# Performance work log

Measured on AMD Instinct MI355X. Metric: run time of the kernel, lower is better.

The kernel has to match this reference:

```python
import jax, jax.numpy as jnp
import numpy as np

B, IMG, D, HEADS, L, PC, PF, OUT = 8, 128, 128, 4, 2, 8, 4, 32
HC = IMG // PC; NC = HC * HC          # 16x16 -> 256 coarse tokens
HF = IMG // PF; NF = HF * HF          # 32x32 -> 1024 fine tokens


def _ln(x, g, b):
    m = x.mean(-1, keepdims=True)
    v = x.var(-1, keepdims=True)
    return (x - m) * jax.lax.rsqrt(v + 1e-5) * g + b


def _conv(x, w, b, pad):
    y = jax.lax.conv_general_dilated(x, w, (1, 1), ((pad, pad), (pad, pad)),
                                     dimension_numbers=('NCHW', 'OIHW', 'NCHW'))
    return y + b[None, :, None, None]


def _bilinear_ac(x, oh, ow):  # F.interpolate(mode='bilinear', align_corners=True)
    _, _, H, W = x.shape
    ys = jnp.linspace(0.0, H - 1.0, oh)
    xs = jnp.linspace(0.0, W - 1.0, ow)
    y0 = jnp.floor(ys).astype(jnp.int32); y1 = jnp.minimum(y0 + 1, H - 1); wy = (ys - y0)[:, None]
    x0 = jnp.floor(xs).astype(jnp.int32); x1 = jnp.minimum(x0 + 1, W - 1); wx = (xs - x0)[None, :]
    g = lambda yi, xi: x[:, :, yi][:, :, :, xi]
    return (g(y0, x0) * (1 - wy) * (1 - wx) + g(y0, x1) * (1 - wy) * wx
            + g(y1, x0) * wy * (1 - wx) + g(y1, x1) * wy * wx)


def _patchify(x, p):  # F.unfold with kernel=stride=p, in_chans=1
    b, _, h, w = x.shape
    return x.reshape(b, h // p, p, w // p, p).transpose(0, 1, 3, 2, 4).reshape(b, (h // p) * (w // p), p * p)


def _forward(x, Wpc, bpc, Wpf, bpf, type_embed, ln1_g, ln1_b, Wqkv, Wo, bo,
             ln2_g, ln2_b, W1, b1, W2, b2, dWc, dbc, dWf, dbf, fW1, fb1, fW2, fb2):
    Bx = x.shape[0]
    # ---- multi-scale patch embed ----
    coarse = _patchify(x, PC) @ Wpc + bpc + type_embed[0]   # [B,NC,D]
    fine = _patchify(x, PF) @ Wpf + bpf                     # [B,NF,D]
    # ---- edge map: sobel -> avgpool(4) -> threshold at per-image mean ----
    gray = x.mean(1, keepdims=True)
    kx = jnp.array([[[[-1, 0, 1], [-2, 0, 2], [-1, 0, 1]]]], x.dtype)
    ky = jnp.array([[[[-1, -2, -1], [0, 0, 0], [1, 2, 1]]]], x.dtype)
    sx = _conv(gray, kx, jnp.zeros((1,), x.dtype), 1)
    sy = _conv(gray, ky, jnp.zeros((1,), x.dtype), 1)
    e = jnp.sqrt(sx ** 2 + sy ** 2)
    e = e.reshape(Bx, 1, IMG // 4, 4, IMG // 4, 4).mean((3, 5))  # [B,1,32,32] == fine grid
    mask_flat = (e > e.mean((2, 3), keepdims=True)).reshape(Bx, NF)
    # ---- static-shape analogue of per-sample masked gather + pad_sequence:
    # stable sort puts edge tokens first (original pixel order preserved), pads are zeros
    order = jnp.argsort(jnp.logical_not(mask_flat), axis=1, stable=True)   # [B,NF]
    mask_sorted = jnp.take_along_axis(mask_flat, order, 1)
    fine_sorted = jnp.take_along_axis(fine, order[..., None], 1) * mask_sorted[..., None]
    fine_sorted = fine_sorted + type_embed[1]   # type embed added to pads too (as in torch)
    tokens = jnp.concatenate([coarse, fine_sorted], axis=1)   # [B,N,D]
    N = NC + NF
    hd = D // HEADS
    scale = hd ** -0.5
    # ---- encoder blocks (pre-LN attn + MLP, irregular-token path) ----
    for l in range(L):
        y = _ln(tokens, ln1_g[l], ln1_b[l])
        qkv = (y @ Wqkv[l]).reshape(Bx, N, 3, HEADS, hd).transpose(2, 0, 3, 1, 4)
        q, k, v = qkv[0], qkv[1], qkv[2]
        attn = jax.nn.softmax(jnp.einsum('bhqd,bhkd->bhqk', q, k) * scale, axis=-1)
        o = jnp.einsum('bhqk,bhkd->bhqd', attn, v).transpose(0, 2, 1, 3).reshape(Bx, N, D)
        tokens = tokens + o @ Wo[l] + bo[l]
        y = _ln(tokens, ln2_g[l], ln2_b[l])
        tokens = tokens + jax.nn.gelu(y @ W1[l] + b1[l], approximate=False) @ W2[l] + b2[l]
    # ---- multi-scale decoder ----
    c = (tokens[:, :NC] @ dWc + dbc).reshape(Bx, HC, HC, 1).transpose(0, 3, 1, 2)
    c_up = _bilinear_ac(c, OUT, OUT)
    feats = (tokens[:, NC:] @ dWf + dbf) * mask_sorted[..., None]   # pads stay zero
    inv = jnp.argsort(order, axis=1)                                # scatter back to pixel order
    f_flat = jnp.take_along_axis(feats, inv[..., None], 1)          # [B,NF,1]
    f_map = f_flat.reshape(Bx, HF, HF, 1).transpose(0, 3, 1, 2)
    f_up = _bilinear_ac(f_map, OUT, OUT)
    fused = jnp.concatenate([c_up, f_up], axis=1)
    h = jax.nn.relu(_conv(fused, fW1, fb1, 1))
    return _conv(h, fW2, fb2, 1)   # [B,1,32,32]


def setup_inputs() -> dict:
    key = jax.random.key(0)
    ks = jax.random.split(key, 16)
    n = lambda k, shape: jax.random.normal(k, shape, jnp.float32) * 0.02
    z = lambda *shape: jnp.zeros(shape, jnp.float32)
    return {
        'x': jax.random.normal(ks[0], (B, 1, IMG, IMG), jnp.float32),
        'Wpc': n(ks[1], (PC * PC, D)), 'bpc': z(D),
        'Wpf': n(ks[2], (PF * PF, D)), 'bpf': z(D),
        'type_embed': n(ks[3], (2, D)),
        'ln1_g': jnp.ones((L, D), jnp.float32), 'ln1_b': z(L, D),
        'Wqkv': n(ks[4], (L, D, 3 * D)),
        'Wo': n(ks[5], (L, D, D)), 'bo': z(L, D),
        'ln2_g': jnp.ones((L, D), jnp.float32), 'ln2_b': z(L, D),
        'W1': n(ks[6], (L, D, 2 * D)), 'b1': z(L, 2 * D),
        'W2': n(ks[7], (L, 2 * D, D)), 'b2': z(L, D),
        'dWc': n(ks[8], (D, 1)), 'dbc': z(1),
        'dWf': n(ks[9], (D, 1)), 'dbf': z(1),
        'fW1': n(ks[10], (2, 2, 3, 3)) * 10.0, 'fb1': z(2),
        'fW2': n(ks[11], (1, 2, 3, 3)) * 10.0, 'fb2': z(1),
    }


def reference(x, Wpc, bpc, Wpf, bpf, type_embed, ln1_g, ln1_b, Wqkv, Wo, bo,
              ln2_g, ln2_b, W1, b1, W2, b2, dWc, dbc, dWf, dbf, fW1, fb1, fW2, fb2):
    return _forward(x, Wpc, bpc, Wpf, bpf, type_embed, ln1_g, ln1_b, Wqkv, Wo, bo,
                    ln2_g, ln2_b, W1, b1, W2, b2, dWc, dbc, dWf, dbf, fW1, fb1, fW2, fb2)
```

## Files before the change

kernel.cpp:

```cpp
#include <hip/hip_runtime.h>
#include <math.h>

#define Bx 8
#define IMG 128
#define DD 128
#define HEADS 4
#define LL 2
#define PCc 8
#define PFf 4
#define HCc 16
#define NCc 256
#define HFf 32
#define NFf 1024
#define NTOK 1280
#define HD 32
#define SPLIT 2
#define NSTG 10
#define NQT 20

typedef __attribute__((ext_vector_type(8))) short short8;
typedef __attribute__((ext_vector_type(4))) float f32x4;

__device__ __forceinline__ short f2bf(float f) {
  unsigned u = __builtin_bit_cast(unsigned, f);
  u += 0x7FFF + ((u >> 16) & 1);
  return (short)(u >> 16);
}
__device__ __forceinline__ float bf2f(short s) {
  unsigned u = ((unsigned)(unsigned short)s) << 16;
  return __builtin_bit_cast(float, u);
}

__global__ __launch_bounds__(256) void k_prologue(const float* __restrict__ x,
    const float* __restrict__ Wpc, const float* __restrict__ bpc,
    const float* __restrict__ Wpf, const float* __restrict__ bpf,
    const float* __restrict__ te,
    const float* __restrict__ Wqkv, const float* __restrict__ Wo,
    const float* __restrict__ W1, const float* __restrict__ W2,
    short* __restrict__ WtQKV, short* __restrict__ WtO,
    short* __restrict__ Wt1, short* __restrict__ Wt2,
    float* __restrict__ e, float* __restrict__ tokens,
    float* __restrict__ fineb) {
  int blk = blockIdx.x;
  int t = threadIdx.x;
  if (blk < 1024) {
    int idx = blk * 256 + t;
    int l = idx / 131072, r = idx % 131072;
    const float* src; short* dst; int N, off;
    if (r < 49152)      { src = Wqkv + l * 49152; dst = WtQKV + l * 49152; N = 384; off = r; }
    else if (r < 65536) { src = Wo + l * 16384;  dst = WtO + l * 16384;  N = 128; off = r - 49152; }
    else if (r < 98304) { src = W1 + l * 32768;  dst = Wt1 + l * 32768;  N = 256; off = r - 65536; }
    else                { src = W2 + l * 32768;  dst = Wt2 + l * 32768;  N = 128; off = r - 98304; }
    int k = off / N, n = off % N;
    int K = (r >= 98304) ? 256 : 128;
    dst[(size_t)n * K + k] = f2bf(src[off]);
  } else if (blk < 1536) {
    int bt = blk - 1024;
    int b = bt >> 6, tile = bt & 63;
    int ty = tile >> 3, tx = tile & 7;
    int ly = t >> 4, lx = t & 15;
    int py = ty * 16 + ly, px = tx * 16 + lx;
    const float* img = x + (size_t)b * IMG * IMG;
    float v[3][3];
    #pragma unroll
    for (int ky = 0; ky < 3; ++ky)
      #pragma unroll
      for (int kx = 0; kx < 3; ++kx) {
        int yy = py + ky - 1, xx = px + kx - 1;
        v[ky][kx] = (yy >= 0 && yy < IMG && xx >= 0 && xx < IMG)
                        ? img[yy * IMG + xx] : 0.f;
      }
    float gx = -v[0][0] + v[0][2] - 2.f * v[1][0] + 2.f * v[1][2] - v[2][0] + v[2][2];
    float gy = -v[0][0] - 2.f * v[0][1] - v[0][2] + v[2][0] + 2.f * v[2][1] + v[2][2];
    __shared__ float sm[256];
    sm[t] = sqrtf(gx * gx + gy * gy);
    __syncthreads();
    if (t < 16) {
      int cy = t >> 2, cx = t & 3;
      float s = 0.f;
      #pragma unroll
      for (int dy = 0; dy < 4; ++dy)
        #pragma unroll
        for (int dx = 0; dx < 4; ++dx) s += sm[(cy * 4 + dy) * 16 + cx * 4 + dx];
      e[b * NFf + (ty * 4 + cy) * 32 + tx * 4 + cx] = s * (1.f / 16.f);
    }
  } else if (blk < 2560) {
    int bt = (blk - 1536) * 2 + (t >> 7);
    int b = bt / NCc, tok = bt % NCc;
    int hc = tok / HCc, wc = tok % HCc;
    int half = t >> 7, d = t & 127;
    __shared__ float patch[2][PCc * PCc];
    if (d < PCc * PCc) {
      int pi = d / PCc, pj = d % PCc;
      patch[half][d] = x[(b * IMG + hc * PCc + pi) * IMG + wc * PCc + pj];
    }
    __syncthreads();
    float acc = bpc[d] + te[d];
    #pragma unroll 8
    for (int i = 0; i < PCc * PCc; ++i) acc += patch[half][i] * Wpc[i * DD + d];
    tokens[(size_t)(b * NTOK + tok) * DD + d] = acc;
  } else {
    int ft = (blk - 2560) * 2 + (t >> 7);
    int b = ft >> 10, tloc = ft & 1023;
    int hf = tloc >> 5, wf = tloc & 31;
    int half = t >> 7, d = t & 127;
    __shared__ float patch[2][PFf * PFf];
    if (d < PFf * PFf) {
      int pi = d / PFf, pj = d % PFf;
      patch[half][d] = x[(b * IMG + hf * PFf + pi) * IMG + wf * PFf + pj];
    }
    __syncthreads();
    float acc = bpf[d];
    #pragma unroll
    for (int i = 0; i < PFf * PFf; ++i) acc += patch[half][i] * Wpf[i * DD + d];
    fineb[(size_t)(b * NFf + tloc) * DD + d] = acc;
  }
}

__global__ __launch_bounds__(1024) void k_edge_sort(const float* __restrict__ e,
    int* __restrict__ order, float* __restrict__ msort) {
  int b = blockIdx.x;
  int t = threadIdx.x;
  int lane = t & 63, wave = t >> 6;
  float ev = e[b * NFf + t];
  __shared__ float wsum[16];
  __shared__ int wcnt[16];
  float r = ev;
  #pragma unroll
  for (int o = 32; o > 0; o >>= 1) r += __shfl_xor(r, o, 64);
  if (lane == 0) wsum[wave] = r;
  __syncthreads();
  float tot = 0.f;
  #pragma unroll
  for (int i = 0; i < 16; ++i) tot += wsum[i];
  float mean = tot * (1.f / 1024.f);
  int m = (ev > mean) ? 1 : 0;
  unsigned long long bal = __ballot(m);
  if (lane == 0) wcnt[wave] = __popcll(bal);
  __syncthreads();
  int wbase = 0, total = 0;
  #pragma unroll
  for (int i = 0; i < 16; ++i) {
    int c = wcnt[i];
    if (i < wave) wbase += c;
    total += c;
  }
  unsigned long long below = (lane == 63) ? ~0ULL : ((1ULL << (lane + 1)) - 1);
  int incl = __popcll(bal & below);
  int eb = wbase + incl - m;
  int pos = m ? eb : (total + t - eb);
  order[b * NFf + pos] = t;
  msort[b * NFf + pos] = (float)m;
}

__global__ __launch_bounds__(256) void k_gather_qkv(float* __restrict__ tokens,
    const float* __restrict__ fineb, const int* __restrict__ order,
    const float* __restrict__ msort, const float* __restrict__ te,
    const float* __restrict__ g, const float* __restrict__ bb,
    const short* __restrict__ WtQ, short* __restrict__ qkvb) {
  __shared__ short Blds[128 * 128];
  __shared__ short Ylds[16 * 136];
  int row0 = blockIdx.x * 16;
  int t = threadIdx.x;
  int lane = t & 63, w = t >> 6;
  int m = lane & 15, quad = lane >> 4;
  int lrow = lane >> 4, jphys = lane & 15;
  f32x4 zero = {0.f, 0.f, 0.f, 0.f};

  #pragma unroll
  for (int j = 0; j < 8; ++j) {
    int c = j * 4 + w;
    int r = c * 4 + lrow;
    int jlog = jphys ^ (r & 15);
    __builtin_amdgcn_global_load_lds(
        (const unsigned*)&WtQ[(size_t)r * 128 + jlog * 8],
        (unsigned*)&Blds[c * 512], 16, 0, 0);
  }
  float2 gg = ((const float2*)g)[lane];
  float2 bv = ((const float2*)bb)[lane];
  #pragma unroll
  for (int rr = 0; rr < 4; ++rr) {
    int lr = w * 4 + rr;
    int row = row0 + lr;
    int b = row / NTOK, rl = row % NTOK;
    float2 v;
    if (rl < NCc) {
      v = ((const float2*)(tokens + (size_t)row * DD))[lane];
    } else {
      int pos = rl - NCc;
      int src = order[b * NFf + pos];
      float mk = msort[b * NFf + pos];
      float2 u = ((const float2*)(fineb + (size_t)(b * NFf + src) * DD))[lane];
      float2 tv = ((const float2*)(te + DD))[lane];
      v.x = u.x * mk + tv.x;
      v.y = u.y * mk + tv.y;
      ((float2*)(tokens + (size_t)row * DD))[lane] = v;
    }
    float s = v.x + v.y;
    #pragma unroll
    for (int o = 32; o > 0; o >>= 1) s += __shfl_xor(s, o, 64);
    float mean = s * (1.f / 128.f);
    float cx = v.x - mean, cy = v.y - mean;
    float q = cx * cx + cy * cy;
    #pragma unroll
    for (int o = 32; o > 0; o >>= 1) q += __shfl_xor(q, o, 64);
    float rstd = rsqrtf(q * (1.f / 128.f) + 1e-5f);
    int p = (int)(unsigned short)f2bf(cx * rstd * gg.x + bv.x)
          | ((int)(unsigned short)f2bf(cy * rstd * gg.y + bv.y) << 16);
    ((int*)Ylds)[lr * 68 + lane] = p;
  }
  for (int c3 = 0; c3 < 3; ++c3) {
    if (c3) {
      __syncthreads();
      #pragma unroll
      for (int j = 0; j < 8; ++j) {
        int c = j * 4 + w;
        int r = c * 4 + lrow;
        int jlog = jphys ^ (r & 15);
        __builtin_amdgcn_global_load_lds(
            (const unsigned*)&WtQ[(size_t)(c3 * 128 + r) * 128 + jlog * 8],
            (unsigned*)&Blds[c * 512], 16, 0, 0);
      }
    }
    __syncthreads();
    f32x4 qa[2] = {zero, zero};
    #pragma unroll
    for (int ks = 0; ks < 4; ++ks) {
      short8 af = *(const short8*)&Ylds[m * 136 + quad * 8 + ks * 32];
      int pc = ((quad + ks * 4) ^ m) * 8;
      #pragma unroll
      for (int nt = 0; nt < 2; ++nt) {
        short8 bf = *(const short8*)&Blds[(w * 32 + nt * 16 + m) * 128 + pc];
        qa[nt] = __builtin_amdgcn_mfma_f32_16x16x32_bf16(af, bf, qa[nt], 0, 0, 0);
      }
    }
    #pragma unroll
    for (int nt = 0; nt < 2; ++nt) {
      int col = c3 * 128 + w * 32 + nt * 16 + m;
      #pragma unroll
      for (int r = 0; r < 4; ++r) {
        int row = row0 + quad * 4 + r;
        qkvb[(size_t)row * 384 + col] = f2bf(qa[nt][r]);
      }
    }
  }
}

__global__ __launch_bounds__(256) void k_fused(const short* __restrict__ Opart,
    const float* __restrict__ Lpart, const short* __restrict__ WtO,
    const float* __restrict__ bo_, const float* __restrict__ ln2g_,
    const float* __restrict__ ln2b_, const short* __restrict__ Wt1,
    const float* __restrict__ b1_, const short* __restrict__ Wt2,
    const float* __restrict__ b2_, float* __restrict__ tokens,
    const float* __restrict__ ln1g_, const float* __restrict__ ln1b_,
    const short* __restrict__ WtQ, short* __restrict__ qkvb,
    const float* __restrict__ dWc_, const float* __restrict__ dbc_,
    const float* __restrict__ dWf_, const float* __restrict__ dbf_,
    float* __restrict__ hrow) {
  __shared__ short Blds[128 * 128];
  __shared__ short AH[16 * 268];
  __shared__ short Ylds[16 * 136];
  __shared__ float pls[4][16], plq[4][16];
  int row0 = blockIdx.x * 16;
  int b = row0 / NTOK;
  int rloc = row0 % NTOK;
  int qt = rloc >> 6, qoff = rloc & 63;
  int t = threadIdx.x;
  int lane = t & 63, w = t >> 6;
  int m = lane & 15, quad = lane >> 4;
  int lrow = lane >> 4, jphys = lane & 15;
  f32x4 zero = {0.f, 0.f, 0.f, 0.f};

  #pragma unroll
  for (int j = 0; j < 8; ++j) {
    int c = j * 4 + w;
    int r = c * 4 + lrow;
    int jlog = jphys ^ (r & 15);
    __builtin_amdgcn_global_load_lds(
        (const unsigned*)&WtO[(size_t)r * 128 + jlog * 8],
        (unsigned*)&Blds[c * 512], 16, 0, 0);
  }
  {
    int q = t >> 4, j = t & 15;
    int dh = j >> 2, dd = (j & 3) * 8;
    int qg = qoff + q;
    size_t pb = ((size_t)(b * HEADS + dh) * NQT + qt) * SPLIT;
    float L = 0.f;
    #pragma unroll
    for (int sk = 0; sk < SPLIT; ++sk) L += Lpart[(pb + sk) * 64 + qg];
    float o[8] = {0, 0, 0, 0, 0, 0, 0, 0};
    #pragma unroll
    for (int sk = 0; sk < SPLIT; ++sk) {
      short8 po = *(const short8*)&Opart[(pb + sk) * 2048 + qg * 32 + dd];
      #pragma unroll
      for (int i = 0; i < 8; ++i) o[i] += bf2f(po[i]);
    }
    float rs = 1.f / L;
    short8 ov;
    #pragma unroll
    for (int i = 0; i < 8; ++i) ov[i] = f2bf(o[i] * rs);
    *(short8*)&AH[q * 136 + j * 8] = ov;
  }
  __syncthreads();
  f32x4 acc[2] = {zero, zero};
  #pragma unroll
  for (int ks = 0; ks < 4; ++ks) {
    short8 af = *(const short8*)&AH[m * 136 + quad * 8 + ks * 32];
    int pc = ((quad + ks * 4) ^ m) * 8;
    #pragma unroll
    for (int nt = 0; nt < 2; ++nt) {
      short8 bf = *(const short8*)&Blds[(w * 32 + nt * 16 + m) * 128 + pc];
      acc[nt] = __builtin_amdgcn_mfma_f32_16x16x32_bf16(af, bf, acc[nt], 0, 0, 0);
    }
  }
  float v[2][4];
  #pragma unroll
  for (int nt = 0; nt < 2; ++nt) {
    int col = w * 32 + nt * 16 + m;
    float bv = bo_[col];
    #pragma unroll
    for (int r = 0; r < 4; ++r) {
      int row = row0 + quad * 4 + r;
      v[nt][r] = acc[nt][r] + bv + tokens[(size_t)row * DD + col];
    }
  }
  #pragma unroll
  for (int r = 0; r < 4; ++r) {
    float s = v[0][r] + v[1][r];
    float q = v[0][r] * v[0][r] + v[1][r] * v[1][r];
    #pragma unroll
    for (int o = 1; o < 16; o <<= 1) { s += __shfl_xor(s, o); q += __shfl_xor(q, o); }
    if (m == 0) {
      int lr = quad * 4 + r;
      pls[w][lr] = s;
      plq[w][lr] = q;
    }
  }
  __syncthreads();
  #pragma unroll
  for (int j = 0; j < 8; ++j) {
    int c = j * 4 + w;
    int r = c * 4 + lrow;
    int jlog = jphys ^ (r & 15);
    __builtin_amdgcn_global_load_lds(
        (const unsigned*)&Wt1[(size_t)r * 128 + jlog * 8],
        (unsigned*)&Blds[c * 512], 16, 0, 0);
  }
  #pragma unroll
  for (int r = 0; r < 4; ++r) {
    int lr = quad * 4 + r;
    float S = pls[0][lr] + pls[1][lr] + pls[2][lr] + pls[3][lr];
    float Q = plq[0][lr] + plq[1][lr] + plq[2][lr] + plq[3][lr];
    float mean = S * (1.f / 128.f);
    float var = Q * (1.f / 128.f) - mean * mean;
    float rstd = rsqrtf(var + 1e-5f);
    #pragma unroll
    for (int nt = 0; nt < 2; ++nt) {
      int col = w * 32 + nt * 16 + m;
      Ylds[lr * 136 + col] = f2bf((v[nt][r] - mean) * rstd * ln2g_[col] + ln2b_[col]);
    }
  }
  for (int hh = 0; hh < 2; ++hh) {
    if (hh) {
      __syncthreads();
      #pragma unroll
      for (int j = 0; j < 8; ++j) {
        int c = j * 4 + w;
        int r = c * 4 + lrow;
        int jlog = jphys ^ (r & 15);
        __builtin_amdgcn_global_load_lds(
            (const unsigned*)&Wt1[(size_t)(128 + r) * 128 + jlog * 8],
            (unsigned*)&Blds[c * 512], 16, 0, 0);
      }
    }
    __syncthreads();
    f32x4 ha[2] = {zero, zero};
    #pragma unroll
    for (int ks = 0; ks < 4; ++ks) {
      short8 af = *(const short8*)&Ylds[m * 136 + quad * 8 + ks * 32];
      int pc = ((quad + ks * 4) ^ m) * 8;
      #pragma unroll
      for (int nt = 0; nt < 2; ++nt) {
        short8 bf = *(const short8*)&Blds[(w * 32 + nt * 16 + m) * 128 + pc];
        ha[nt] = __builtin_amdgcn_mfma_f32_16x16x32_bf16(af, bf, ha[nt], 0, 0, 0);
      }
    }
    #pragma unroll
    for (int nt = 0; nt < 2; ++nt) {
      int n = hh * 128 + w * 32 + nt * 16 + m;
      float bv = b1_[n];
      #pragma unroll
      for (int r = 0; r < 4; ++r) {
        float vv = ha[nt][r] + bv;
        vv = 0.5f * vv * (1.f + erff(vv * 0.70710678118654752f));
        AH[(quad * 4 + r) * 268 + n] = f2bf(vv);
      }
    }
  }
  f32x4 a2[2] = {zero, zero};
  for (int kb = 0; kb < 2; ++kb) {
    __syncthreads();
    #pragma unroll
    for (int j = 0; j < 8; ++j) {
      int c = j * 4 + w;
      int r = c * 4 + lrow;
      int jlog = jphys ^ (r & 15);
      __builtin_amdgcn_global_load_lds(
          (const unsigned*)&Wt2[(size_t)r * 256 + kb * 128 + jlog * 8],
          (unsigned*)&Blds[c * 512], 16, 0, 0);
    }
    __syncthreads();
    #pragma unroll
    for (int ks = 0; ks < 4; ++ks) {
      int pc = ((quad + ks * 4) ^ m) * 8;
      short8 af = *(const short8*)&AH[m * 268 + kb * 128 + quad * 8 + ks * 32];
      #pragma unroll
      for (int nt = 0; nt < 2; ++nt) {
        short8 bf = *(const short8*)&Blds[(w * 32 + nt * 16 + m) * 128 + pc];
        a2[nt] = __builtin_amdgcn_mfma_f32_16x16x32_bf16(af, bf, a2[nt], 0, 0, 0);
      }
    }
  }
  #pragma unroll
  for (int nt = 0; nt < 2; ++nt) {
    int col = w * 32 + nt * 16 + m;
    float bv = b2_[col];
    #pragma unroll
    for (int r = 0; r < 4; ++r) {
      int row = row0 + quad * 4 + r;
      float val = a2[nt][r] + bv + v[nt][r];
      tokens[(size_t)row * DD + col] = val;
      v[nt][r] = val;
    }
  }
  if (ln1g_ == nullptr) {
    bool coarse = (rloc < NCc);
    const float* dw = coarse ? dWc_ : dWf_;
    float dwv[2];
    #pragma unroll
    for (int nt = 0; nt < 2; ++nt) dwv[nt] = dw[w * 32 + nt * 16 + m];
    #pragma unroll
    for (int r = 0; r < 4; ++r) {
      float s = v[0][r] * dwv[0] + v[1][r] * dwv[1];
      #pragma unroll
      for (int o = 1; o < 16; o <<= 1) s += __shfl_xor(s, o);
      if (m == 0) pls[w][quad * 4 + r] = s;
    }
    __syncthreads();
    if (m == 0 && w == 0) {
      float dbv = coarse ? dbc_[0] : dbf_[0];
      #pragma unroll
      for (int r = 0; r < 4; ++r) {
        int lr = quad * 4 + r;
        hrow[row0 + lr] = pls[0][lr] + pls[1][lr] + pls[2][lr] + pls[3][lr] + dbv;
      }
    }
    return;
  }
  #pragma unroll
  for (int r = 0; r < 4; ++r) {
    float s = v[0][r] + v[1][r];
    float q = v[0][r] * v[0][r] + v[1][r] * v[1][r];
    #pragma unroll
    for (int o = 1; o < 16; o <<= 1) { s += __shfl_xor(s, o); q += __shfl_xor(q, o); }
    if (m == 0) {
      int lr = quad * 4 + r;
      pls[w][lr] = s;
      plq[w][lr] = q;
    }
  }
  __syncthreads();
  #pragma unroll
  for (int j = 0; j < 8; ++j) {
    int c = j * 4 + w;
    int r = c * 4 + lrow;
    int jlog = jphys ^ (r & 15);
    __builtin_amdgcn_global_load_lds(
        (const unsigned*)&WtQ[(size_t)r * 128 + jlog * 8],
        (unsigned*)&Blds[c * 512], 16, 0, 0);
  }
  #pragma unroll
  for (int r = 0; r < 4; ++r) {
    int lr = quad * 4 + r;
    float S = pls[0][lr] + pls[1][lr] + pls[2][lr] + pls[3][lr];
    float Q = plq[0][lr] + plq[1][lr] + plq[2][lr] + plq[3][lr];
    float mean = S * (1.f / 128.f);
    float var = Q * (1.f / 128.f) - mean * mean;
    float rstd = rsqrtf(var + 1e-5f);
    #pragma unroll
    for (int nt = 0; nt < 2; ++nt) {
      int col = w * 32 + nt * 16 + m;
      Ylds[lr * 136 + col] = f2bf((v[nt][r] - mean) * rstd * ln1g_[col] + ln1b_[col]);
    }
  }
  for (int c3 = 0; c3 < 3; ++c3) {
    if (c3) {
      __syncthreads();
      #pragma unroll
      for (int j = 0; j < 8; ++j) {
        int c = j * 4 + w;
        int r = c * 4 + lrow;
        int jlog = jphys ^ (r & 15);
        __builtin_amdgcn_global_load_lds(
            (const unsigned*)&WtQ[(size_t)(c3 * 128 + r) * 128 + jlog * 8],
            (unsigned*)&Blds[c * 512], 16, 0, 0);
      }
    }
    __syncthreads();
    f32x4 qa[2] = {zero, zero};
    #pragma unroll
    for (int ks = 0; ks < 4; ++ks) {
      short8 af = *(const short8*)&Ylds[m * 136 + quad * 8 + ks * 32];
      int pc = ((quad + ks * 4) ^ m) * 8;
      #pragma unroll
      for (int nt = 0; nt < 2; ++nt) {
        short8 bf = *(const short8*)&Blds[(w * 32 + nt * 16 + m) * 128 + pc];
        qa[nt] = __builtin_amdgcn_mfma_f32_16x16x32_bf16(af, bf, qa[nt], 0, 0, 0);
      }
    }
    #pragma unroll
    for (int nt = 0; nt < 2; ++nt) {
      int col = c3 * 128 + w * 32 + nt * 16 + m;
      #pragma unroll
      for (int r = 0; r < 4; ++r) {
        int row = row0 + quad * 4 + r;
        qkvb[(size_t)row * 384 + col] = f2bf(qa[nt][r]);
      }
    }
  }
}

__global__ __launch_bounds__(256) void k_attn4(const short* __restrict__ qkv,
    short* __restrict__ Opart, float* __restrict__ Lpart) {
  __shared__ short Ks[2][64 * 32];
  __shared__ short Vt[2][32 * 74];
  __shared__ short Pl[4][16 * 74];

  int hid = blockIdx.x;
  int g = hid & 31;
  int k = hid >> 5;
  int b = g >> 2, h = g & 3;
  int qt = k / SPLIT, sk = k % SPLIT;
  size_t lid = ((size_t)g * NQT + qt) * SPLIT + sk;
  int t = threadIdx.x;
  int lane = t & 63, w = t >> 6;
  int m = lane & 15, quad = lane >> 4;
  int q0 = qt * 64 + w * 16;

  const float scale = 0.17677669529663687f;
  short8 qraw = *(const short8*)(qkv + ((size_t)(b * NTOK) + q0 + m) * 384 + h * HD + quad * 8);
  short8 qf;
  #pragma unroll
  for (int j = 0; j < 8; ++j) qf[j] = f2bf(bf2f(qraw[j]) * scale);

  f32x4 zero = {0.f, 0.f, 0.f, 0.f};
  f32x4 Oacc[2] = {zero, zero};
  float psum[4] = {0.f, 0.f, 0.f, 0.f};

  int skey = t >> 2, sdseg = t & 3;
  int jlogK = sdseg ^ ((skey >> 1) & 3);
  const short* kstage = qkv + ((size_t)(b * NTOK) + skey) * 384 + 128 + h * HD + jlogK * 8;
  const short* vstage = qkv + ((size_t)(b * NTOK) + skey) * 384 + 256 + h * HD + sdseg * 8;
  int kswz = (quad ^ ((m >> 1) & 3)) * 8;

  int s0 = sk * NSTG;
  __builtin_amdgcn_global_load_lds((const unsigned*)(kstage + (size_t)s0 * 64 * 384),
                                   (unsigned*)&Ks[0][w * 512], 16, 0, 0);
  {
    short8 vf = *(const short8*)(vstage + (size_t)s0 * 64 * 384);
    #pragma unroll
    for (int j = 0; j < 8; ++j) Vt[0][(sdseg * 8 + j) * 74 + skey] = vf[j];
  }
  __syncthreads();

  for (int i = 0; i < NSTG; ++i) {
    int cur = i & 1;
    short8 vf;
    if (i + 1 < NSTG) {
      __builtin_amdgcn_global_load_lds(
          (const unsigned*)(kstage + (size_t)(s0 + i + 1) * 64 * 384),
          (unsigned*)&Ks[cur ^ 1][w * 512], 16, 0, 0);
      vf = *(const short8*)(vstage + (size_t)(s0 + i + 1) * 64 * 384);
    }

    f32x4 sc[4];
    #pragma unroll
    for (int ct = 0; ct < 4; ++ct) {
      short8 kfrag = *(const short8*)&Ks[cur][(ct * 16 + m) * 32 + kswz];
      sc[ct] = __builtin_amdgcn_mfma_f32_16x16x32_bf16(qf, kfrag, zero, 0, 0, 0);
    }
    #pragma unroll
    for (int ct = 0; ct < 4; ++ct)
      #pragma unroll
      for (int r = 0; r < 4; ++r) {
        float p = __expf(sc[ct][r]);
        unsigned u = __builtin_bit_cast(unsigned, p);
        psum[r] += __builtin_bit_cast(float, u & 0xffff0000u);
        Pl[w][(quad * 4 + r) * 74 + ct * 16 + m] = (short)(u >> 16);
      }
    #pragma unroll
    for (int ks = 0; ks < 2; ++ks) {
      short8 pfrag = *(const short8*)&Pl[w][m * 74 + ks * 32 + quad * 8];
      #pragma unroll
      for (int nt = 0; nt < 2; ++nt) {
        short8 vfrag = *(const short8*)&Vt[cur][(nt * 16 + m) * 74 + ks * 32 + quad * 8];
        Oacc[nt] = __builtin_amdgcn_mfma_f32_16x16x32_bf16(pfrag, vfrag, Oacc[nt], 0, 0, 0);
      }
    }
    if (i + 1 < NSTG) {
      #pragma unroll
      for (int j = 0; j < 8; ++j) Vt[cur ^ 1][(sdseg * 8 + j) * 74 + skey] = vf[j];
    }
    __syncthreads();
  }
  #pragma unroll
  for (int r = 0; r < 4; ++r) {
    float ssum = psum[r];
    #pragma unroll
    for (int o = 1; o < 16; o <<= 1) ssum += __shfl_xor(ssum, o);
    int qloc = w * 16 + quad * 4 + r;
    #pragma unroll
    for (int nt = 0; nt < 2; ++nt)
      Opart[lid * 2048 + qloc * 32 + nt * 16 + m] = f2bf(Oacc[nt][r]);
    if (m == 0) Lpart[lid * 64 + qloc] = ssum;
  }
}

__global__ __launch_bounds__(1024) void k_decoder(const float* __restrict__ hrow,
    const float* __restrict__ msort, const int* __restrict__ order,
    const float* __restrict__ fW1, const float* __restrict__ fb1,
    const float* __restrict__ fW2, const float* __restrict__ fb2,
    float* __restrict__ outp) {
  int b = blockIdx.x;
  int t = threadIdx.x;
  __shared__ float cmap[NCc];
  __shared__ float fmap[1024];
  __shared__ float cup[1024];
  __shared__ float hb[2][1024];
  fmap[order[b * NFf + t]] = hrow[b * NTOK + NCc + t] * msort[b * NFf + t];
  if (t < NCc) cmap[t] = hrow[b * NTOK + t];
  __syncthreads();
  int y = t >> 5, x = t & 31;
  {
    float ys = y * (15.f / 31.f);
    float xs = x * (15.f / 31.f);
    int y0 = (int)floorf(ys); int y1 = min(y0 + 1, 15); float wy = ys - (float)y0;
    int x0 = (int)floorf(xs); int x1 = min(x0 + 1, 15); float wx = xs - (float)x0;
    cup[t] = cmap[y0 * 16 + x0] * (1.f - wy) * (1.f - wx)
           + cmap[y0 * 16 + x1] * (1.f - wy) * wx
           + cmap[y1 * 16 + x0] * wy * (1.f - wx)
           + cmap[y1 * 16 + x1] * wy * wx;
  }
  __syncthreads();
  for (int oc = 0; oc < 2; ++oc) {
    float a = fb1[oc];
    #pragma unroll
    for (int ic = 0; ic < 2; ++ic)
      #pragma unroll
      for (int ky = 0; ky < 3; ++ky)
        #pragma unroll
        for (int kx = 0; kx < 3; ++kx) {
          int yy = y + ky - 1, xx = x + kx - 1;
          float v = 0.f;
          if (yy >= 0 && yy < 32 && xx >= 0 && xx < 32)
            v = ic == 0 ? cup[yy * 32 + xx] : fmap[yy * 32 + xx];
          a += v * fW1[((oc * 2 + ic) * 3 + ky) * 3 + kx];
        }
    hb[oc][t] = fmaxf(a, 0.f);
  }
  __syncthreads();
  float a = fb2[0];
  #pragma unroll
  for (int ic = 0; ic < 2; ++ic)
    #pragma unroll
    for (int ky = 0; ky < 3; ++ky)
      #pragma unroll
      for (int kx = 0; kx < 3; ++kx) {
        int yy = y + ky - 1, xx = x + kx - 1;
        float v = (yy >= 0 && yy < 32 && xx >= 0 && xx < 32)
                      ? hb[ic][yy * 32 + xx] : 0.f;
        a += v * fW2[(ic * 3 + ky) * 3 + kx];
      }
  outp[b * 1024 + t] = a;
}

extern "C" void kernel_launch(void* const* d_in, const int* in_sizes, int n_in,
                              void* d_out, int out_size, void* d_ws, size_t ws_size,
                              hipStream_t stream) {
  const float* x    = (const float*)d_in[0];
  const float* Wpc  = (const float*)d_in[1];
  const float* bpc  = (const float*)d_in[2];
  const float* Wpf  = (const float*)d_in[3];
  const float* bpf  = (const float*)d_in[4];
  const float* te   = (const float*)d_in[5];
  const float* ln1g = (const float*)d_in[6];
  const float* ln1b = (const float*)d_in[7];
  const float* Wqkv = (const float*)d_in[8];
  const float* Wo   = (const float*)d_in[9];
  const float* bo   = (const float*)d_in[10];
  const float* ln2g = (const float*)d_in[11];
  const float* ln2b = (const float*)d_in[12];
  const float* W1   = (const float*)d_in[13];
  const float* b1   = (const float*)d_in[14];
  const float* W2   = (const float*)d_in[15];
  const float* b2   = (const float*)d_in[16];
  const float* dWc  = (const float*)d_in[17];
  const float* dbc  = (const float*)d_in[18];
  const float* dWf  = (const float*)d_in[19];
  const float* dbf  = (const float*)d_in[20];
  const float* fW1  = (const float*)d_in[21];
  const float* fb1  = (const float*)d_in[22];
  const float* fW2  = (const float*)d_in[23];
  const float* fb2  = (const float*)d_in[24];

  char* ws = (char*)d_ws;
  float* tokens = (float*)ws;                 ws += 1310720 * 4;
  float* fineb  = (float*)ws;                 ws += 1048576 * 4;
  short* qkvb   = (short*)ws;                 ws += 3932160 * 2;
  short* Opart  = (short*)ws;                 ws += (size_t)(Bx * HEADS * NQT * SPLIT) * 2048 * 2;
  float* Lpart  = (float*)ws;                 ws += (size_t)(Bx * HEADS * NQT * SPLIT) * 64 * 4;
  short* WtQKV  = (short*)ws;                 ws += 98304 * 2;
  short* WtO    = (short*)ws;                 ws += 32768 * 2;
  short* Wt1    = (short*)ws;                 ws += 65536 * 2;
  short* Wt2    = (short*)ws;                 ws += 65536 * 2;
  float* ebuf   = (float*)ws;                 ws += 8192 * 4;
  float* msort  = (float*)ws;                 ws += 8192 * 4;
  int*   order  = (int*)ws;                   ws += 8192 * 4;
  float* hrow   = (float*)ws;                 ws += 10240 * 4;

  const int M = Bx * NTOK;

  k_prologue<<<6656, 256, 0, stream>>>(x, Wpc, bpc, Wpf, bpf, te, Wqkv, Wo, W1, W2,
                                       WtQKV, WtO, Wt1, Wt2, ebuf, tokens, fineb);
  k_edge_sort<<<Bx, 1024, 0, stream>>>(ebuf, order, msort);
  k_gather_qkv<<<M / 16, 256, 0, stream>>>(tokens, fineb, order, msort, te,
                                           ln1g, ln1b, WtQKV, qkvb);

  k_attn4<<<Bx * HEADS * NQT * SPLIT, 256, 0, stream>>>(qkvb, Opart, Lpart);
  k_fused<<<M / 16, 256, 0, stream>>>(
      Opart, Lpart, WtO, bo, ln2g, ln2b,
      Wt1, b1, Wt2, b2, tokens,
      ln1g + DD, ln1b + DD, WtQKV + 49152, qkvb,
      nullptr, nullptr, nullptr, nullptr, nullptr);

  k_attn4<<<Bx * HEADS * NQT * SPLIT, 256, 0, stream>>>(qkvb, Opart, Lpart);
  k_fused<<<M / 16, 256, 0, stream>>>(
      Opart, Lpart, WtO + 16384, bo + DD, ln2g + DD, ln2b + DD,
      Wt1 + 32768, b1 + 256, Wt2 + 32768, b2 + DD, tokens,
      nullptr, nullptr, nullptr, nullptr,
      dWc, dbc, dWf, dbf, hrow);

  k_decoder<<<Bx, 1024, 0, stream>>>(hrow, msort, order,
                                     fW1, fb1, fW2, fb2, (float*)d_out);
}
```

Measured before the change: 214.3 us.

## Read MFMA weight fragments directly from global memory instead of staging in LDS

Removes the shared-memory staging of the QKV, output-projection and MLP weight tiles in the gather and fused kernels. MFMA B fragments are now loaded straight from global memory and rely on L2/L1 caching, since every 16-row block rereads the same small weights. This drops the 32 KB LDS buffer and most of the barriers, which should raise occupancy and cut sync stalls. The residual tokens are also loaded early into registers. The cost is global-load latency on the MFMA critical path and more traffic through the vector cache.

Result: slower. 237.7 us (+10.9%).

```diff
diff --git a/kernel.cpp b/kernel.cpp
--- a/kernel.cpp
+++ b/kernel.cpp
@@ -158,24 +158,13 @@
     const float* __restrict__ msort, const float* __restrict__ te,
     const float* __restrict__ g, const float* __restrict__ bb,
     const short* __restrict__ WtQ, short* __restrict__ qkvb) {
-  __shared__ short Blds[128 * 128];
   __shared__ short Ylds[16 * 136];
   int row0 = blockIdx.x * 16;
   int t = threadIdx.x;
   int lane = t & 63, w = t >> 6;
   int m = lane & 15, quad = lane >> 4;
-  int lrow = lane >> 4, jphys = lane & 15;
   f32x4 zero = {0.f, 0.f, 0.f, 0.f};
 
-  #pragma unroll
-  for (int j = 0; j < 8; ++j) {
-    int c = j * 4 + w;
-    int r = c * 4 + lrow;
-    int jlog = jphys ^ (r & 15);
-    __builtin_amdgcn_global_load_lds(
-        (const unsigned*)&WtQ[(size_t)r * 128 + jlog * 8],
-        (unsigned*)&Blds[c * 512], 16, 0, 0);
-  }
   float2 gg = ((const float2*)g)[lane];
   float2 bv = ((const float2*)bb)[lane];
   #pragma unroll
@@ -209,28 +198,16 @@
           | ((int)(unsigned short)f2bf(cy * rstd * gg.y + bv.y) << 16);
     ((int*)Ylds)[lr * 68 + lane] = p;
   }
+  __syncthreads();
   for (int c3 = 0; c3 < 3; ++c3) {
-    if (c3) {
-      __syncthreads();
-      #pragma unroll
-      for (int j = 0; j < 8; ++j) {
-        int c = j * 4 + w;
-        int r = c * 4 + lrow;
-        int jlog = jphys ^ (r & 15);
-        __builtin_amdgcn_global_load_lds(
-            (const unsigned*)&WtQ[(size_t)(c3 * 128 + r) * 128 + jlog * 8],
-            (unsigned*)&Blds[c * 512], 16, 0, 0);
-      }
-    }
-    __syncthreads();
     f32x4 qa[2] = {zero, zero};
     #pragma unroll
     for (int ks = 0; ks < 4; ++ks) {
       short8 af = *(const short8*)&Ylds[m * 136 + quad * 8 + ks * 32];
-      int pc = ((quad + ks * 4) ^ m) * 8;
       #pragma unroll
       for (int nt = 0; nt < 2; ++nt) {
-        short8 bf = *(const short8*)&Blds[(w * 32 + nt * 16 + m) * 128 + pc];
+        short8 bf = *(const short8*)&WtQ[(size_t)(c3 * 128 + w * 32 + nt * 16 + m) * 128
+                                         + (quad + ks * 4) * 8];
         qa[nt] = __builtin_amdgcn_mfma_f32_16x16x32_bf16(af, bf, qa[nt], 0, 0, 0);
       }
     }
@@ -257,7 +234,6 @@
     const float* __restrict__ dWc_, const float* __restrict__ dbc_,
     const float* __restrict__ dWf_, const float* __restrict__ dbf_,
     float* __restrict__ hrow) {
-  __shared__ short Blds[128 * 128];
   __shared__ short AH[16 * 268];
   __shared__ short Ylds[16 * 136];
   __shared__ float pls[4][16], plq[4][16];
@@ -268,17 +244,15 @@
   int t = threadIdx.x;
   int lane = t & 63, w = t >> 6;
   int m = lane & 15, quad = lane >> 4;
-  int lrow = lane >> 4, jphys = lane & 15;
   f32x4 zero = {0.f, 0.f, 0.f, 0.f};
 
-  #pragma unroll
-  for (int j = 0; j < 8; ++j) {
-    int c = j * 4 + w;
-    int r = c * 4 + lrow;
-    int jlog = jphys ^ (r & 15);
-    __builtin_amdgcn_global_load_lds(
-        (const unsigned*)&WtO[(size_t)r * 128 + jlog * 8],
-        (unsigned*)&Blds[c * 512], 16, 0, 0);
+  float res[2][4];
+  #pragma unroll
+  for (int nt = 0; nt < 2; ++nt) {
+    int col = w * 32 + nt * 16 + m;
+    #pragma unroll
+    for (int r = 0; r < 4; ++r)
+      res[nt][r] = tokens[(size_t)(row0 + quad * 4 + r) * DD + col];
   }
   {
     int q = t >> 4, j = t & 15;
@@ -306,10 +280,10 @@
   #pragma unroll
   for (int ks = 0; ks < 4; ++ks) {
     short8 af = *(const short8*)&AH[m * 136 + quad * 8 + ks * 32];
-    int pc = ((quad + ks * 4) ^ m) * 8;
     #pragma unroll
     for (int nt = 0; nt < 2; ++nt) {
-      short8 bf = *(const short8*)&Blds[(w * 32 + nt * 16 + m) * 128 + pc];
+      short8 bf = *(const short8*)&WtO[(size_t)(w * 32 + nt * 16 + m) * 128
+                                       + (quad + ks * 4) * 8];
       acc[nt] = __builtin_amdgcn_mfma_f32_16x16x32_bf16(af, bf, acc[nt], 0, 0, 0);
     }
   }
@@ -319,10 +293,8 @@
     int col = w * 32 + nt * 16 + m;
     float bv = bo_[col];
     #pragma unroll
-    for (int r = 0; r < 4; ++r) {
-      int row = row0 + quad * 4 + r;
-      v[nt][r] = acc[nt][r] + bv + tokens[(size_t)row * DD + col];
-    }
+    for (int r = 0; r < 4; ++r)
+      v[nt][r] = acc[nt][r] + bv + res[nt][r];
   }
   #pragma unroll
   for (int r = 0; r < 4; ++r) {
@@ -337,15 +309,6 @@
     }
   }
   __syncthreads();
-  #pragma unroll
-  for (int j = 0; j < 8; ++j) {
-    int c = j * 4 + w;
-    int r = c * 4 + lrow;
-    int jlog = jphys ^ (r & 15);
-    __builtin_amdgcn_global_load_lds(
-        (const unsigned*)&Wt1[(size_t)r * 128 + jlog * 8],
-        (unsigned*)&Blds[c * 512], 16, 0, 0);
-  }
   #pragma unroll
   for (int r = 0; r < 4; ++r) {
     int lr = quad * 4 + r;
@@ -360,28 +323,16 @@
       Ylds[lr * 136 + col] = f2bf((v[nt][r] - mean) * rstd * ln2g_[col] + ln2b_[col]);
     }
   }
+  __syncthreads();
   for (int hh = 0; hh < 2; ++hh) {
-    if (hh) {
-      __syncthreads();
-      #pragma unroll
-      for (int j = 0; j < 8; ++j) {
-        int c = j * 4 + w;
-        int r = c * 4 + lrow;
-        int jlog = jphys ^ (r & 15);
-        __builtin_amdgcn_global_load_lds(
-            (const unsigned*)&Wt1[(size_t)(128 + r) * 128 + jlog * 8],
-            (unsigned*)&Blds[c * 512], 16, 0, 0);
-      }
-    }
-    __syncthreads();
     f32x4 ha[2] = {zero, zero};
     #pragma unroll
     for (int ks = 0; ks < 4; ++ks) {
       short8 af = *(const short8*)&Ylds[m * 136 + quad * 8 + ks * 32];
-      int pc = ((quad + ks * 4) ^ m) * 8;
       #pragma unroll
       for (int nt = 0; nt < 2; ++nt) {
-        short8 bf = *(const short8*)&Blds[(w * 32 + nt * 16 + m) * 128 + pc];
+        short8 bf = *(const short8*)&Wt1[(size_t)(hh * 128 + w * 32 + nt * 16 + m) * 128
+                                         + (quad + ks * 4) * 8];
         ha[nt] = __builtin_amdgcn_mfma_f32_16x16x32_bf16(af, bf, ha[nt], 0, 0, 0);
       }
     }
@@ -397,26 +348,17 @@
       }
     }
   }
+  __syncthreads();
   f32x4 a2[2] = {zero, zero};
+  #pragma unroll
   for (int kb = 0; kb < 2; ++kb) {
-    __syncthreads();
-    #pragma unroll
-    for (int j = 0; j < 8; ++j) {
-      int c = j * 4 + w;
-      int r = c * 4 + lrow;
-      int jlog = jphys ^ (r & 15);
-      __builtin_amdgcn_global_load_lds(
-          (const unsigned*)&Wt2[(size_t)r * 256 + kb * 128 + jlog * 8],
-          (unsigned*)&Blds[c * 512], 16, 0, 0);
-    }
-    __syncthreads();
     #pragma unroll
     for (int ks = 0; ks < 4; ++ks) {
-      int pc = ((quad + ks * 4) ^ m) * 8;
       short8 af = *(const short8*)&AH[m * 268 + kb * 128 + quad * 8 + ks * 32];
       #pragma unroll
       for (int nt = 0; nt < 2; ++nt) {
-        short8 bf = *(const short8*)&Blds[(w * 32 + nt * 16 + m) * 128 + pc];
+        short8 bf = *(const short8*)&Wt2[(size_t)(w * 32 + nt * 16 + m) * 256
+                                         + kb * 128 + (quad + ks * 4) * 8];
         a2[nt] = __builtin_amdgcn_mfma_f32_16x16x32_bf16(af, bf, a2[nt], 0, 0, 0);
       }
     }
@@ -470,15 +412,6 @@
     }
   }
   __syncthreads();
-  #pragma unroll
-  for (int j = 0; j < 8; ++j) {
-    int c = j * 4 + w;
-    int r = c * 4 + lrow;
-    int jlog = jphys ^ (r & 15);
-    __builtin_amdgcn_global_load_lds(
-        (const unsigned*)&WtQ[(size_t)r * 128 + jlog * 8],
-        (unsigned*)&Blds[c * 512], 16, 0, 0);
-  }
   #pragma unroll
   for (int r = 0; r < 4; ++r) {
     int lr = quad * 4 + r;
@@ -493,28 +426,16 @@
       Ylds[lr * 136 + col] = f2bf((v[nt][r] - mean) * rstd * ln1g_[col] + ln1b_[col]);
     }
   }
+  __syncthreads();
   for (int c3 = 0; c3 < 3; ++c3) {
-    if (c3) {
-      __syncthreads();
-      #pragma unroll
-      for (int j = 0; j < 8; ++j) {
-        int c = j * 4 + w;
-        int r = c * 4 + lrow;
-        int jlog = jphys ^ (r & 15);
-        __builtin_amdgcn_global_load_lds(
-            (const unsigned*)&WtQ[(size_t)(c3 * 128 + r) * 128 + jlog * 8],
-            (unsigned*)&Blds[c * 512], 16, 0, 0);
-      }
-    }
-    __syncthreads();
     f32x4 qa[2] = {zero, zero};
     #pragma unroll
     for (int ks = 0; ks < 4; ++ks) {
       short8 af = *(const short8*)&Ylds[m * 136 + quad * 8 + ks * 32];
-      int pc = ((quad + ks * 4) ^ m) * 8;
       #pragma unroll
       for (int nt = 0; nt < 2; ++nt) {
-        short8 bf = *(const short8*)&Blds[(w * 32 + nt * 16 + m) * 128 + pc];
+        short8 bf = *(const short8*)&WtQ[(size_t)(c3 * 128 + w * 32 + nt * 16 + m) * 128
+                                         + (quad + ks * 4) * 8];
         qa[nt] = __builtin_amdgcn_mfma_f32_16x16x32_bf16(af, bf, qa[nt], 0, 0, 0);
       }
     }
```
